# Optimization experiments

Hardware: AMD Instinct MI355X
Metric: run time of the kernel (lower is better)

## Reference

```python
import jax, jax.numpy as jnp
import numpy as np

N = 50000
E = 800000
NODE_IN = 128
HID = 256
OUT = 256
EDGE_DIM = 16
HEADS = 4
CH = HID // HEADS  # 64
NEG_SLOPE = 0.2


def _init_linear(key, fan_in, fan_out):
    k1, k2 = jax.random.split(key)
    bound = 1.0 / np.sqrt(fan_in)
    W = jax.random.uniform(k1, (fan_in, fan_out), jnp.float32, -bound, bound)
    b = jax.random.uniform(k2, (fan_out,), jnp.float32, -bound, bound)
    return W, b


def setup_inputs() -> dict:
    key = jax.random.key(0)
    ks = jax.random.split(key, 12)
    node_feats = jax.random.normal(ks[0], (N, NODE_IN), jnp.float32)
    edge_index = jax.random.randint(ks[1], (2, E), 0, N, jnp.int64)
    edge_attr = jax.random.normal(ks[2], (E, EDGE_DIM), jnp.float32)

    Wnp, bnp = _init_linear(ks[3], NODE_IN, HID)           # node_proj
    Wep, bep = _init_linear(ks[4], EDGE_DIM, HID)          # edge_proj
    # GATConv 1: in = 2*HID, out per head = CH
    Wg1, _ = _init_linear(ks[5], 2 * HID, HEADS * CH)
    as1 = jax.random.normal(ks[6], (HEADS, CH), jnp.float32) * 0.1
    ad1 = jax.random.normal(ks[7], (HEADS, CH), jnp.float32) * 0.1
    bg1 = jnp.zeros((HEADS * CH,), jnp.float32)
    # GATConv 2: in = HID, out per head = OUT//HEADS
    Wg2, _ = _init_linear(ks[8], HID, HEADS * (OUT // HEADS))
    as2 = jax.random.normal(ks[9], (HEADS, OUT // HEADS), jnp.float32) * 0.1
    ad2 = jax.random.normal(ks[10], (HEADS, OUT // HEADS), jnp.float32) * 0.1
    bg2 = jnp.zeros((OUT,), jnp.float32)
    Wo, bo = _init_linear(ks[11], OUT, OUT)                # out_proj
    return {
        "node_feats": node_feats, "edge_attr": edge_attr,
        "Wnp": Wnp, "bnp": bnp, "Wep": Wep, "bep": bep,
        "Wg1": Wg1, "as1": as1, "ad1": ad1, "bg1": bg1,
        "Wg2": Wg2, "as2": as2, "ad2": ad2, "bg2": bg2,
        "Wo": Wo, "bo": bo,
        "edge_index": edge_index,
    }


def scatter_mean(src, index, num_nodes):
    # mean of edge features grouped by target node; empty groups -> 0 (count clamped to 1)
    s = jax.ops.segment_sum(src, index, num_segments=num_nodes)
    cnt = jax.ops.segment_sum(jnp.ones((src.shape[0],), src.dtype), index, num_segments=num_nodes)
    return s / jnp.maximum(cnt, 1.0)[:, None]


def gat_conv(x, src, dst, W, att_src, att_dst, bias, num_nodes, heads, ch):
    # PyG GATConv with add_self_loops=True (loops appended by caller via src/dst),
    # concat=True, negative_slope=0.2.
    xh = (x @ W).reshape(num_nodes, heads, ch)             # [N,H,C]
    a_src = jnp.sum(xh * att_src, axis=-1)                 # [N,H]
    a_dst = jnp.sum(xh * att_dst, axis=-1)                 # [N,H]
    logits = jax.nn.leaky_relu(a_src[src] + a_dst[dst], NEG_SLOPE)  # [E,H]
    # segment softmax over incoming edges of each destination node
    m = jax.ops.segment_max(logits, dst, num_segments=num_nodes)    # [N,H]
    ex = jnp.exp(logits - m[dst])
    denom = jax.ops.segment_sum(ex, dst, num_segments=num_nodes)    # [N,H]
    alpha = ex / denom[dst]                                          # [E,H]
    msg = xh[src] * alpha[:, :, None]                                # [E,H,C]
    out = jax.ops.segment_sum(msg, dst, num_segments=num_nodes)      # [N,H,C]
    return out.reshape(num_nodes, heads * ch) + bias


def reference(node_feats, edge_attr, Wnp, bnp, Wep, bep,
              Wg1, as1, ad1, bg1, Wg2, as2, ad2, bg2, Wo, bo, edge_index):
    n = node_feats.shape[0]
    x = node_feats @ Wnp + bnp                                       # [N,HID]
    # EdgeAggregator: mean of edge_attr over target nodes, then edge_proj
    nef = scatter_mean(edge_attr, edge_index[1], n)                  # [N,EDGE_DIM]
    nef = nef @ Wep + bep                                            # [N,HID]
    x = jnp.concatenate([x, nef], axis=-1)                           # [N,2*HID]
    # add self loops once (same augmented edge set for both GAT layers)
    loops = jnp.arange(n, dtype=edge_index.dtype)
    src = jnp.concatenate([edge_index[0], loops])
    dst = jnp.concatenate([edge_index[1], loops])
    x = jax.nn.elu(gat_conv(x, src, dst, Wg1, as1, ad1, bg1, n, HEADS, CH))
    # dropout is identity in eval mode
    x = jax.nn.elu(gat_conv(x, src, dst, Wg2, as2, ad2, bg2, n, HEADS, OUT // HEADS))
    return x @ Wo + bo
```

## Files before the change

kernel.cpp:

```cpp
#include <hip/hip_runtime.h>
#include <hip/hip_bf16.h>


#define HEADS 4

typedef __attribute__((ext_vector_type(8))) _Float16 f16x8;
typedef __attribute__((ext_vector_type(4))) float f32x4;
typedef __attribute__((ext_vector_type(4))) unsigned short u16x4;
typedef __attribute__((ext_vector_type(8))) unsigned short u16x8;

__device__ __forceinline__ unsigned short f2h(float v) {
    _Float16 h = (_Float16)v;
    return __builtin_bit_cast(unsigned short, h);
}
__device__ __forceinline__ float h2f(unsigned short u) {
    return (float)__builtin_bit_cast(_Float16, u);
}
__device__ __forceinline__ void split_hilo16(float v, unsigned short& h, unsigned short& l) {
    h = f2h(v);
    l = f2h(v - h2f(h));
}
__device__ __forceinline__ void gl2lds16(const unsigned short* g, unsigned short* l) {
    __builtin_amdgcn_global_load_lds(
        (const __attribute__((address_space(1))) unsigned int*)g,
        (__attribute__((address_space(3))) unsigned int*)l,
        16, 0, 0);
}


__global__ __launch_bounds__(256) void count_kernel(
    const int* __restrict__ dst, int* __restrict__ cnt, int E)
{
    int e = blockIdx.x * 256 + threadIdx.x;
    if (e < E) atomicAdd(&cnt[dst[e]], 1);
}

__global__ __launch_bounds__(256) void scan1_kernel(
    const int* __restrict__ cnt, int* __restrict__ chunk_sum, int N)
{
    __shared__ int sd[256];
    int t = threadIdx.x;
    int n = blockIdx.x * 256 + t;
    sd[t] = (n < N) ? (cnt[n] + 1) : 0;
    __syncthreads();
    for (int o = 128; o > 0; o >>= 1) {
        if (t < o) sd[t] += sd[t + o];
        __syncthreads();
    }
    if (t == 0) chunk_sum[blockIdx.x] = sd[0];
}

__global__ __launch_bounds__(256) void scan2_kernel(
    const int* __restrict__ chunk_sum, int* __restrict__ chunk_off, int nchunk)
{
    __shared__ int sd[256];
    __shared__ int carry;
    int t = threadIdx.x;
    if (t == 0) carry = 0;
    __syncthreads();
    for (int b = 0; b < nchunk; b += 256) {
        int i = b + t;
        int v = (i < nchunk) ? chunk_sum[i] : 0;
        sd[t] = v;
        __syncthreads();
        for (int o = 1; o < 256; o <<= 1) {
            int x = (t >= o) ? sd[t - o] : 0;
            __syncthreads();
            sd[t] += x;
            __syncthreads();
        }
        if (i < nchunk) chunk_off[i] = carry + sd[t] - v;
        __syncthreads();
        if (t == 0) carry += sd[255];
        __syncthreads();
    }
}

__global__ __launch_bounds__(256) void scan3_kernel(
    const int* __restrict__ cnt, const int* __restrict__ chunk_off,
    int* __restrict__ rowptr, int* __restrict__ fillptr,
    int* __restrict__ col, int* __restrict__ eid, int N)
{
    __shared__ int sd[256];
    int t = threadIdx.x;
    int n = blockIdx.x * 256 + t;
    int v = (n < N) ? (cnt[n] + 1) : 0;
    sd[t] = v;
    __syncthreads();
    for (int o = 1; o < 256; o <<= 1) {
        int x = (t >= o) ? sd[t - o] : 0;
        __syncthreads();
        sd[t] += x;
        __syncthreads();
    }
    if (n < N) {
        int incl = sd[t];
        int r = chunk_off[blockIdx.x] + incl - v;
        rowptr[n] = r;
        col[r] = n;
        eid[r] = -1;
        fillptr[n] = r + 1;
        if (n == N - 1) rowptr[N] = chunk_off[blockIdx.x] + incl;
    }
}

__global__ __launch_bounds__(256) void fill_kernel(
    const int* __restrict__ src, const int* __restrict__ dst,
    int* __restrict__ fillptr, int* __restrict__ col, int* __restrict__ eid, int E)
{
    int e = blockIdx.x * 256 + threadIdx.x;
    if (e >= E) return;
    int d = dst[e];
    int p = atomicAdd(&fillptr[d], 1);
    col[p] = src[e];
    eid[p] = e;
}

__global__ __launch_bounds__(256) void nef_csr_kernel(
    const float* __restrict__ ea, const int* __restrict__ rowptr,
    const int* __restrict__ eid,
    unsigned short* __restrict__ AF, int N)
{
    int n = blockIdx.x * 4 + (threadIdx.x >> 6);
    if (n >= N) return;
    int t = threadIdx.x & 63;
    int f = t & 15, g = t >> 4;
    int base = rowptr[n], end = rowptr[n + 1];
    int deg = end - base - 1;
    float acc = 0.0f;
    for (int j = base + 1 + g; j < end; j += 4) {
        int e = eid[j];
        acc += ea[(size_t)e * 16 + f];
    }
    acc += __shfl_down(acc, 32, 64);
    acc += __shfl_down(acc, 16, 64);
    if (t < 16) {
        float v = acc / fmaxf((float)deg, 1.0f);
        AF[(size_t)n * 160 + 128 + t] = f2h(v);
    } else if (t < 32) {
        AF[(size_t)n * 160 + 128 + t] = 0;
    }
}

__global__ __launch_bounds__(256) void conv_f16_strided_kernel(
    const float* __restrict__ X, unsigned short* __restrict__ AF, int total)
{
    int base = (blockIdx.x * 256 + threadIdx.x) * 2;
    if (base >= total) return;
    #pragma unroll
    for (int i = 0; i < 2; i++) {
        int e = base + i;
        int row = e >> 7, c = e & 127;
        AF[(size_t)row * 160 + c] = f2h(X[e]);
    }
}

__global__ __launch_bounds__(256) void compose_w1_kernel(
    const float* __restrict__ Wnp, const float* __restrict__ Wep,
    const float* __restrict__ bnp, const float* __restrict__ bep,
    const float* __restrict__ Wg1,
    float* __restrict__ Wc, float* __restrict__ c1)
{
    int idx = blockIdx.x * 256 + threadIdx.x;
    if (idx >= 145 * 256) return;
    int i = idx >> 8, j = idx & 255;
    float s = 0.0f;
    if (i < 128) {
        for (int k = 0; k < 256; k++) s += Wnp[i * 256 + k] * Wg1[(size_t)k * 256 + j];
        Wc[i * 256 + j] = s;
    } else if (i < 144) {
        int ii = i - 128;
        for (int k = 0; k < 256; k++) s += Wep[ii * 256 + k] * Wg1[(size_t)(256 + k) * 256 + j];
        Wc[i * 256 + j] = s;
    } else {
        for (int k = 0; k < 256; k++)
            s += bnp[k] * Wg1[(size_t)k * 256 + j] + bep[k] * Wg1[(size_t)(256 + k) * 256 + j];
        c1[j] = s;
    }
}

__device__ __forceinline__ void pack_one(
    const float* __restrict__ W, int K, int KP, int idx,
    unsigned short* __restrict__ Ph, unsigned short* __restrict__ Pl)
{
    int tile = idx >> 9, w = idx & 511, lane = w >> 3, j = w & 7;
    int nk = KP >> 5;
    int ctile = tile / nk, t = tile % nk;
    int k = t * 32 + ((lane >> 4) << 3) + j;
    int n = (ctile << 4) + (lane & 15);
    float v = (k < K) ? W[(size_t)k * 256 + n] : 0.0f;
    unsigned short h, l;
    split_hilo16(v, h, l);
    Ph[idx] = h;
    Pl[idx] = l;
}

__global__ __launch_bounds__(256) void pack3_w_kernel(
    const float* __restrict__ Wc,  unsigned short* __restrict__ PcH,  unsigned short* __restrict__ PcL,
    const float* __restrict__ Wg2, unsigned short* __restrict__ Pg2H, unsigned short* __restrict__ Pg2L,
    const float* __restrict__ Wo,  unsigned short* __restrict__ PoH,  unsigned short* __restrict__ PoL)
{
    const int S0 = 160 * 256;
    const int S1 = S0 + 256 * 256;
    const int S2 = S1 + 256 * 256;
    int idx = blockIdx.x * 256 + threadIdx.x;
    if (idx < S0) {
        pack_one(Wc, 144, 160, idx, PcH, PcL);
    } else if (idx < S1) {
        pack_one(Wg2, 256, 256, idx - S0, Pg2H, Pg2L);
    } else if (idx < S2) {
        pack_one(Wo, 256, 256, idx - S1, PoH, PoL);
    }
}

template <int KSTEPS, int AMODE, int OMODE, bool FUSE_ATT>
__global__ __launch_bounds__(256, 5) void mfma_gemm_kernel(
    const unsigned short* __restrict__ Ah, const unsigned short* __restrict__ Al,
    int lda,
    const unsigned short* __restrict__ Ph, const unsigned short* __restrict__ Pl,
    const float* __restrict__ bias,
    float* __restrict__ Cf,
    unsigned short* __restrict__ Ch, unsigned short* __restrict__ Cl,
    int ldc, int col_off, int Nrows,
    const float* __restrict__ att_src, const float* __restrict__ att_dst,
    float* __restrict__ a_srcO, float* __restrict__ a_dstO)
{
    __shared__ unsigned short ldsB[2][2][8][512];
    int tid = threadIdx.x;
    int wave = tid >> 6, lane = tid & 63;
    int quad = lane >> 4, m16 = lane & 15;
    int rowblk = blockIdx.x, colhalf = blockIdx.y;
    int ctile0 = colhalf * 8;

    int row = rowblk * 64 + wave * 16 + m16;
    bool rowok = row < Nrows;
    const unsigned short* arh = Ah + (size_t)row * lda;
    const unsigned short* arl = (AMODE == 0) ? (Al + (size_t)row * lda) : nullptr;

    auto stage = [&](int t, int buf) {
        #pragma unroll
        for (int q = 0; q < 2; q++) {
            int c = wave * 2 + q;
            size_t gb = ((size_t)((ctile0 + c) * KSTEPS + t)) * 512 + lane * 8;
            gl2lds16(Ph + gb, &ldsB[buf][0][c][0]);
            gl2lds16(Pl + gb, &ldsB[buf][1][c][0]);
        }
    };
    auto loadA = [&](int t, f16x8& h, f16x8& l) {
        int k = t * 32 + quad * 8;
        h = (f16x8){};
        l = (f16x8){};
        if (rowok) {
            h = __builtin_bit_cast(f16x8, *(const u16x8*)(arh + k));
            if (AMODE == 0)
                l = __builtin_bit_cast(f16x8, *(const u16x8*)(arl + k));
        }
    };

    f32x4 acc[8] = {};
    f16x8 ah2[2], al2[2];
    loadA(0, ah2[0], al2[0]);
    stage(0, 0);
    __syncthreads();

    #pragma unroll
    for (int t = 0; t < KSTEPS; t++) {
        const int buf = t & 1;
        if (t + 1 < KSTEPS) {
            stage(t + 1, buf ^ 1);
            loadA(t + 1, ah2[(t + 1) & 1], al2[(t + 1) & 1]);
        }
        #pragma unroll
        for (int c = 0; c < 8; c++) {
            f16x8 b_h = __builtin_bit_cast(f16x8, *(const u16x8*)&ldsB[buf][0][c][lane * 8]);
            f16x8 b_l = __builtin_bit_cast(f16x8, *(const u16x8*)&ldsB[buf][1][c][lane * 8]);
            acc[c] = __builtin_amdgcn_mfma_f32_16x16x32_f16(ah2[buf], b_h, acc[c], 0, 0, 0);
            if (AMODE == 0)
                acc[c] = __builtin_amdgcn_mfma_f32_16x16x32_f16(al2[buf], b_h, acc[c], 0, 0, 0);
            acc[c] = __builtin_amdgcn_mfma_f32_16x16x32_f16(ah2[buf], b_l, acc[c], 0, 0, 0);
        }
        if (t + 1 < KSTEPS) __syncthreads();
    }

    #pragma unroll
    for (int c = 0; c < 8; c++) {
        int ocol = (ctile0 + c) * 16 + m16;
        float bv = bias ? bias[ocol] : 0.0f;
        #pragma unroll
        for (int r = 0; r < 4; r++) {
            int orow = rowblk * 64 + wave * 16 + quad * 4 + r;
            if (orow >= Nrows) continue;
            float v = acc[c][r] + bv;
            size_t oidx = (size_t)orow * ldc + col_off + ocol;
            if (OMODE == 1) {
                unsigned short h, l;
                split_hilo16(v, h, l);
                Ch[oidx] = h;
                Cl[oidx] = l;
            } else if (OMODE == 2) {
                Ch[oidx] = f2h(v);
            } else {
                Cf[oidx] = v;
            }
        }
    }

    if (FUSE_ATT) {
        float ps[4][2] = {}, pd[4][2] = {};
        #pragma unroll
        for (int c = 0; c < 8; c++) {
            int ocol = (ctile0 + c) * 16 + m16;
            float bv = bias ? bias[ocol] : 0.0f;
            float asv = att_src[ocol];
            float adv = att_dst[ocol];
            int hl = c >> 2;
            #pragma unroll
            for (int r = 0; r < 4; r++) {
                float v = acc[c][r] + bv;
                ps[r][hl] += v * asv;
                pd[r][hl] += v * adv;
            }
        }
        #pragma unroll
        for (int r = 0; r < 4; r++) {
            #pragma unroll
            for (int hl = 0; hl < 2; hl++) {
                float s = ps[r][hl], d = pd[r][hl];
                #pragma unroll
                for (int o = 8; o > 0; o >>= 1) {
                    s += __shfl_down(s, o, 64);
                    d += __shfl_down(d, o, 64);
                }
                if (m16 == 0) {
                    int orow = rowblk * 64 + wave * 16 + quad * 4 + r;
                    if (orow < Nrows) {
                        int gh = colhalf * 2 + hl;
                        a_srcO[orow * 4 + gh] = s;
                        a_dstO[orow * 4 + gh] = d;
                    }
                }
            }
        }
    }
}

template <bool OUTF16>
__global__ __launch_bounds__(256) void gat_agg_csr_kernel(
    const unsigned short* __restrict__ xh,
    const int* __restrict__ rowptr, const int* __restrict__ col,
    const float* __restrict__ a_src, const float* __restrict__ a_dst,
    const float* __restrict__ bias,
    unsigned short* __restrict__ outA, unsigned short* __restrict__ outB, int N)
{
    __shared__ float wlds[4][128][HEADS];
    int t = threadIdx.x;
    int wv = t >> 6;
    int n = blockIdx.x * 4 + wv;
    if (n >= N) return;
    int c = t & 63;
    int h = c >> 4;
    int base = rowptr[n], end = rowptr[n + 1];
    int deg = end - base;
    int e1 = end - 1;
    float4 ad = *(const float4*)&a_dst[n * 4];
    float adh = (h == 0) ? ad.x : (h == 1) ? ad.y : (h == 2) ? ad.z : ad.w;
    const unsigned short* xcol = xh + (c << 2);

    float4 acc = {0.0f, 0.0f, 0.0f, 0.0f};
    float den = 0.0f;

    if (deg <= 128) {
        float4 ds = {0.0f, 0.0f, 0.0f, 0.0f};
        for (int j = base + c; j < end; j += 64) {
            int s = col[j];
            float4 as4 = *(const float4*)&a_src[s * 4];
            float l0 = as4.x + ad.x, l1 = as4.y + ad.y;
            float l2 = as4.z + ad.z, l3 = as4.w + ad.w;
            l0 = fmaxf(l0, 0.2f * l0);
            l1 = fmaxf(l1, 0.2f * l1);
            l2 = fmaxf(l2, 0.2f * l2);
            l3 = fmaxf(l3, 0.2f * l3);
            float4 wv4 = {__expf(l0), __expf(l1), __expf(l2), __expf(l3)};
            *(float4*)&wlds[wv][j - base][0] = wv4;
            ds.x += wv4.x; ds.y += wv4.y; ds.z += wv4.z; ds.w += wv4.w;
        }
        #pragma unroll
        for (int o = 32; o > 0; o >>= 1) {
            ds.x += __shfl_down(ds.x, o, 64);
            ds.y += __shfl_down(ds.y, o, 64);
            ds.z += __shfl_down(ds.z, o, 64);
            ds.w += __shfl_down(ds.w, o, 64);
        }
        float d0 = __shfl(ds.x, 0, 64);
        float d1 = __shfl(ds.y, 0, 64);
        float d2 = __shfl(ds.z, 0, 64);
        float d3 = __shfl(ds.w, 0, 64);
        den = (h == 0) ? d0 : (h == 1) ? d1 : (h == 2) ? d2 : d3;

        for (int j = base; j < end; j += 4) {
            int j1 = j + 1 < e1 ? j + 1 : e1;
            int j2 = j + 2 < e1 ? j + 2 : e1;
            int j3 = j + 3 < e1 ? j + 3 : e1;
            int s0 = col[j], s1 = col[j1], s2 = col[j2], s3 = col[j3];
            float w0 = wlds[wv][j - base][h];
            float w1 = (j + 1 < end) ? wlds[wv][j1 - base][h] : 0.0f;
            float w2 = (j + 2 < end) ? wlds[wv][j2 - base][h] : 0.0f;
            float w3 = (j + 3 < end) ? wlds[wv][j3 - base][h] : 0.0f;
            u16x4 x0 = *(const u16x4*)(xcol + (size_t)s0 * 256);
            u16x4 x1 = *(const u16x4*)(xcol + (size_t)s1 * 256);
            u16x4 x2 = *(const u16x4*)(xcol + (size_t)s2 * 256);
            u16x4 x3 = *(const u16x4*)(xcol + (size_t)s3 * 256);
            acc.x += w0 * h2f(x0[0]) + w1 * h2f(x1[0]) + w2 * h2f(x2[0]) + w3 * h2f(x3[0]);
            acc.y += w0 * h2f(x0[1]) + w1 * h2f(x1[1]) + w2 * h2f(x2[1]) + w3 * h2f(x3[1]);
            acc.z += w0 * h2f(x0[2]) + w1 * h2f(x1[2]) + w2 * h2f(x2[2]) + w3 * h2f(x3[2]);
            acc.w += w0 * h2f(x0[3]) + w1 * h2f(x1[3]) + w2 * h2f(x2[3]) + w3 * h2f(x3[3]);
        }
    } else {
        for (int j = base; j < end; j += 4) {
            int j1 = j + 1 < e1 ? j + 1 : e1;
            int j2 = j + 2 < e1 ? j + 2 : e1;
            int j3 = j + 3 < e1 ? j + 3 : e1;
            int s0 = col[j], s1 = col[j1], s2 = col[j2], s3 = col[j3];
            float l0 = a_src[s0 * 4 + h] + adh;
            float l1 = a_src[s1 * 4 + h] + adh;
            float l2 = a_src[s2 * 4 + h] + adh;
            float l3 = a_src[s3 * 4 + h] + adh;
            l0 = fmaxf(l0, 0.2f * l0);
            l1 = fmaxf(l1, 0.2f * l1);
            l2 = fmaxf(l2, 0.2f * l2);
            l3 = fmaxf(l3, 0.2f * l3);
            float w0 = __expf(l0);
            float w1 = (j + 1 < end) ? __expf(l1) : 0.0f;
            float w2 = (j + 2 < end) ? __expf(l2) : 0.0f;
            float w3 = (j + 3 < end) ? __expf(l3) : 0.0f;
            u16x4 x0 = *(const u16x4*)(xcol + (size_t)s0 * 256);
            u16x4 x1 = *(const u16x4*)(xcol + (size_t)s1 * 256);
            u16x4 x2 = *(const u16x4*)(xcol + (size_t)s2 * 256);
            u16x4 x3 = *(const u16x4*)(xcol + (size_t)s3 * 256);
            den += (w0 + w1) + (w2 + w3);
            acc.x += w0 * h2f(x0[0]) + w1 * h2f(x1[0]) + w2 * h2f(x2[0]) + w3 * h2f(x3[0]);
            acc.y += w0 * h2f(x0[1]) + w1 * h2f(x1[1]) + w2 * h2f(x2[1]) + w3 * h2f(x3[1]);
            acc.z += w0 * h2f(x0[2]) + w1 * h2f(x1[2]) + w2 * h2f(x2[2]) + w3 * h2f(x3[2]);
            acc.w += w0 * h2f(x0[3]) + w1 * h2f(x1[3]) + w2 * h2f(x2[3]) + w3 * h2f(x3[3]);
        }
    }

    float inv = 1.0f / den;
    float4 bv = *(const float4*)(bias + (c << 2));
    float o0 = acc.x * inv + bv.x;
    float o1 = acc.y * inv + bv.y;
    float o2 = acc.z * inv + bv.z;
    float o3 = acc.w * inv + bv.w;
    o0 = (o0 > 0.0f) ? o0 : (__expf(o0) - 1.0f);
    o1 = (o1 > 0.0f) ? o1 : (__expf(o1) - 1.0f);
    o2 = (o2 > 0.0f) ? o2 : (__expf(o2) - 1.0f);
    o3 = (o3 > 0.0f) ? o3 : (__expf(o3) - 1.0f);
    if (OUTF16) {
        u16x4 H;
        H[0] = f2h(o0); H[1] = f2h(o1); H[2] = f2h(o2); H[3] = f2h(o3);
        *(u16x4*)(&outA[(size_t)n * 256 + (c << 2)]) = H;
    } else {
        u16x4 H, L;
        split_hilo16(o0, ((unsigned short*)&H)[0], ((unsigned short*)&L)[0]);
        split_hilo16(o1, ((unsigned short*)&H)[1], ((unsigned short*)&L)[1]);
        split_hilo16(o2, ((unsigned short*)&H)[2], ((unsigned short*)&L)[2]);
        split_hilo16(o3, ((unsigned short*)&H)[3], ((unsigned short*)&L)[3]);
        *(u16x4*)(&outA[(size_t)n * 256 + (c << 2)]) = H;
        *(u16x4*)(&outB[(size_t)n * 256 + (c << 2)]) = L;
    }
}


extern "C" void kernel_launch(void* const* d_in, const int* in_sizes, int n_in,
                              void* d_out, int out_size, void* d_ws, size_t ws_size,
                              hipStream_t stream)
{
    const float* node_feats = (const float*)d_in[0];
    const float* edge_attr  = (const float*)d_in[1];
    const float* Wnp = (const float*)d_in[2];
    const float* bnp = (const float*)d_in[3];
    const float* Wep = (const float*)d_in[4];
    const float* bep = (const float*)d_in[5];
    const float* Wg1 = (const float*)d_in[6];
    const float* as1 = (const float*)d_in[7];
    const float* ad1 = (const float*)d_in[8];
    const float* bg1 = (const float*)d_in[9];
    const float* Wg2 = (const float*)d_in[10];
    const float* as2 = (const float*)d_in[11];
    const float* ad2 = (const float*)d_in[12];
    const float* bg2 = (const float*)d_in[13];
    const float* Wo  = (const float*)d_in[14];
    const float* bo  = (const float*)d_in[15];
    const int*   ei  = (const int*)d_in[16];

    const int N = in_sizes[0] / 128;
    const int E = in_sizes[16] / 2;
    const int* src = ei;
    const int* dst = ei + E;
    const int nchunk = (N + 255) / 256;
    const int EN = E + N;

    typedef unsigned short u16;

    char* base = (char*)d_ws;
    size_t off = 0;
    auto alloc = [&](size_t bytes) -> char* {
        char* p = base + off;
        off += (bytes + 255) & ~(size_t)255;
        return p;
    };
    u16* xhh = (u16*)alloc((size_t)N * 256 * 2);
    u16* R2  = (u16*)alloc((size_t)N * 512 * 2);
    u16* R3  = (u16*)alloc((size_t)N * 512 * 2);
    float* a_src = (float*)alloc((size_t)N * 4 * 4);
    float* a_dst = (float*)alloc((size_t)N * 4 * 4);
    float* Wc    = (float*)alloc(144 * 256 * 4);
    float* c1    = (float*)alloc(256 * 4);
    u16* PcH  = (u16*)alloc(160 * 256 * 2);
    u16* PcL  = (u16*)alloc(160 * 256 * 2);
    u16* Pg2H = (u16*)alloc(256 * 256 * 2);
    u16* Pg2L = (u16*)alloc(256 * 256 * 2);
    u16* PoH  = (u16*)alloc(256 * 256 * 2);
    u16* PoL  = (u16*)alloc(256 * 256 * 2);
    int* cnt       = (int*)alloc((size_t)N * 4);
    int* rowptr    = (int*)alloc((size_t)(N + 1) * 4);
    int* fillptr   = (int*)alloc((size_t)N * 4);
    int* chunk_sum = (int*)alloc((size_t)nchunk * 4);
    int* chunk_off = (int*)alloc((size_t)nchunk * 4);
    int* colv      = (int*)alloc((size_t)EN * 4);
    int* eid       = (int*)alloc((size_t)EN * 4);

    u16* AcatF = R2;
    u16* x3F   = R2;
    u16* x4H = R3;
    u16* x4L = R3 + (size_t)N * 256;

    float* out = (float*)d_out;
    dim3 ggrid((N + 63) / 64, 2);

    hipMemsetAsync(cnt, 0, (size_t)N * sizeof(int), stream);
    count_kernel<<<(E + 255) / 256, 256, 0, stream>>>(dst, cnt, E);
    scan1_kernel<<<nchunk, 256, 0, stream>>>(cnt, chunk_sum, N);
    scan2_kernel<<<1, 256, 0, stream>>>(chunk_sum, chunk_off, nchunk);
    scan3_kernel<<<nchunk, 256, 0, stream>>>(cnt, chunk_off, rowptr, fillptr, colv, eid, N);
    fill_kernel<<<(E + 255) / 256, 256, 0, stream>>>(src, dst, fillptr, colv, eid, E);

    nef_csr_kernel<<<(N + 3) / 4, 256, 0, stream>>>(edge_attr, rowptr, eid, AcatF, N);
    conv_f16_strided_kernel<<<((N * 128) / 2 + 255) / 256, 256, 0, stream>>>(
        node_feats, AcatF, N * 128);
    compose_w1_kernel<<<145, 256, 0, stream>>>(Wnp, Wep, bnp, bep, Wg1, Wc, c1);
    {
        const int total = 160 * 256 + 256 * 256 + 256 * 256;
        pack3_w_kernel<<<(total + 255) / 256, 256, 0, stream>>>(
            Wc, PcH, PcL, Wg2, Pg2H, Pg2L, Wo, PoH, PoL);
    }

    mfma_gemm_kernel<5, 1, 2, true><<<ggrid, 256, 0, stream>>>(
        AcatF, nullptr, 160, PcH, PcL, c1, nullptr, xhh, nullptr, 256, 0, N,
        as1, ad1, a_src, a_dst);
    gat_agg_csr_kernel<true><<<(N + 3) / 4, 256, 0, stream>>>(
        xhh, rowptr, colv, a_src, a_dst, bg1, x3F, nullptr, N);

    mfma_gemm_kernel<8, 1, 2, true><<<ggrid, 256, 0, stream>>>(
        x3F, nullptr, 256, Pg2H, Pg2L, nullptr, nullptr, xhh, nullptr, 256, 0, N,
        as2, ad2, a_src, a_dst);
    gat_agg_csr_kernel<false><<<(N + 3) / 4, 256, 0, stream>>>(
        xhh, rowptr, colv, a_src, a_dst, bg2, x4H, x4L, N);

    mfma_gemm_kernel<8, 0, 0, false><<<ggrid, 256, 0, stream>>>(
        x4H, x4L, 256, PoH, PoL, bo, out, nullptr, nullptr, 256, 0, N,
        nullptr, nullptr, nullptr, nullptr);
}
```

Before: 539.0 us.

## Fuse fp32-to-fp16 input conversion into first GEMM and preload A fragments

Removes the separate conversion kernel that wrote node features as fp16 into a strided concat buffer. The first GEMM now reads fp32 node features directly and converts them in registers, and reads edge-mean features from a small separate buffer. All GEMMs now preload every A fragment for the whole K range into registers up front, and launch bounds drop to 4 blocks per SM to make room. This saves a full write-and-read pass over the feature matrix, at the cost of more registers and lower occupancy in all GEMMs.

New measurement: 533.1 us (median of 2 runs). About the same (-1.1%).

```diff
diff --git a/kernel.cpp b/kernel.cpp
--- a/kernel.cpp
+++ b/kernel.cpp
@@ -119,7 +119,7 @@
 __global__ __launch_bounds__(256) void nef_csr_kernel(
     const float* __restrict__ ea, const int* __restrict__ rowptr,
     const int* __restrict__ eid,
-    unsigned short* __restrict__ AF, int N)
+    unsigned short* __restrict__ nefF, int N)
 {
     int n = blockIdx.x * 4 + (threadIdx.x >> 6);
     if (n >= N) return;
@@ -136,22 +136,9 @@
     acc += __shfl_down(acc, 16, 64);
     if (t < 16) {
         float v = acc / fmaxf((float)deg, 1.0f);
-        AF[(size_t)n * 160 + 128 + t] = f2h(v);
+        nefF[(size_t)n * 32 + t] = f2h(v);
     } else if (t < 32) {
-        AF[(size_t)n * 160 + 128 + t] = 0;
-    }
-}
-
-__global__ __launch_bounds__(256) void conv_f16_strided_kernel(
-    const float* __restrict__ X, unsigned short* __restrict__ AF, int total)
-{
-    int base = (blockIdx.x * 256 + threadIdx.x) * 2;
-    if (base >= total) return;
-    #pragma unroll
-    for (int i = 0; i < 2; i++) {
-        int e = base + i;
-        int row = e >> 7, c = e & 127;
-        AF[(size_t)row * 160 + c] = f2h(X[e]);
+        nefF[(size_t)n * 32 + t] = 0;
     }
 }
 
@@ -214,8 +201,9 @@
 }
 
 template <int KSTEPS, int AMODE, int OMODE, bool FUSE_ATT>
-__global__ __launch_bounds__(256, 5) void mfma_gemm_kernel(
+__global__ __launch_bounds__(256, 4) void mfma_gemm_kernel(
     const unsigned short* __restrict__ Ah, const unsigned short* __restrict__ Al,
+    const float* __restrict__ Af32,
     int lda,
     const unsigned short* __restrict__ Ph, const unsigned short* __restrict__ Pl,
     const float* __restrict__ bias,
@@ -234,8 +222,6 @@
 
     int row = rowblk * 64 + wave * 16 + m16;
     bool rowok = row < Nrows;
-    const unsigned short* arh = Ah + (size_t)row * lda;
-    const unsigned short* arl = (AMODE == 0) ? (Al + (size_t)row * lda) : nullptr;
 
     auto stage = [&](int t, int buf) {
         #pragma unroll
@@ -246,38 +232,65 @@
             gl2lds16(Pl + gb, &ldsB[buf][1][c][0]);
         }
     };
-    auto loadA = [&](int t, f16x8& h, f16x8& l) {
-        int k = t * 32 + quad * 8;
-        h = (f16x8){};
-        l = (f16x8){};
-        if (rowok) {
-            h = __builtin_bit_cast(f16x8, *(const u16x8*)(arh + k));
-            if (AMODE == 0)
-                l = __builtin_bit_cast(f16x8, *(const u16x8*)(arl + k));
-        }
-    };
+
+    u16x8 aH[KSTEPS];
+    u16x8 aL[AMODE == 0 ? KSTEPS : 1];
+    f32x4 aF[AMODE == 3 ? 2 * KSTEPS : 1];
+    #pragma unroll
+    for (int t = 0; t < KSTEPS; t++) {
+        if (AMODE == 3) {
+            if (t < KSTEPS - 1) {
+                aF[2 * t] = (f32x4){};
+                aF[2 * t + 1] = (f32x4){};
+                if (rowok) {
+                    const float* p = Af32 + (size_t)row * 128 + t * 32 + quad * 8;
+                    aF[2 * t]     = *(const f32x4*)p;
+                    aF[2 * t + 1] = *(const f32x4*)(p + 4);
+                }
+            } else {
+                aH[t] = (u16x8){};
+                if (rowok) aH[t] = *(const u16x8*)(Ah + (size_t)row * 32 + quad * 8);
+            }
+        } else {
+            int k = t * 32 + quad * 8;
+            aH[t] = (u16x8){};
+            if (rowok) aH[t] = *(const u16x8*)(Ah + (size_t)row * lda + k);
+            if (AMODE == 0) {
+                aL[t] = (u16x8){};
+                if (rowok) aL[t] = *(const u16x8*)(Al + (size_t)row * lda + k);
+            }
+        }
+    }
 
     f32x4 acc[8] = {};
-    f16x8 ah2[2], al2[2];
-    loadA(0, ah2[0], al2[0]);
     stage(0, 0);
     __syncthreads();
 
     #pragma unroll
     for (int t = 0; t < KSTEPS; t++) {
         const int buf = t & 1;
-        if (t + 1 < KSTEPS) {
-            stage(t + 1, buf ^ 1);
-            loadA(t + 1, ah2[(t + 1) & 1], al2[(t + 1) & 1]);
-        }
+        if (t + 1 < KSTEPS) stage(t + 1, buf ^ 1);
+
+        f16x8 a_h, a_l;
+        if (AMODE == 3 && t < KSTEPS - 1) {
+            #pragma unroll
+            for (int i = 0; i < 4; i++) {
+                ((_Float16*)&a_h)[i]     = (_Float16)aF[2 * t][i];
+                ((_Float16*)&a_h)[4 + i] = (_Float16)aF[2 * t + 1][i];
+            }
+        } else {
+            a_h = __builtin_bit_cast(f16x8, aH[t]);
+        }
+        if (AMODE == 0) a_l = __builtin_bit_cast(f16x8, aL[t]);
+
         #pragma unroll
         for (int c = 0; c < 8; c++) {
             f16x8 b_h = __builtin_bit_cast(f16x8, *(const u16x8*)&ldsB[buf][0][c][lane * 8]);
             f16x8 b_l = __builtin_bit_cast(f16x8, *(const u16x8*)&ldsB[buf][1][c][lane * 8]);
-            acc[c] = __builtin_amdgcn_mfma_f32_16x16x32_f16(ah2[buf], b_h, acc[c], 0, 0, 0);
+            acc[c] = __builtin_amdgcn_mfma_f32_16x16x32_f16(a_h, b_h, acc[c], 0, 0, 0);
             if (AMODE == 0)
-                acc[c] = __builtin_amdgcn_mfma_f32_16x16x32_f16(al2[buf], b_h, acc[c], 0, 0, 0);
-            acc[c] = __builtin_amdgcn_mfma_f32_16x16x32_f16(ah2[buf], b_l, acc[c], 0, 0, 0);
+                acc[c] = __builtin_amdgcn_mfma_f32_16x16x32_f16(a_l, b_h, acc[c], 0, 0, 0);
+            acc[c] = __builtin_amdgcn_mfma_f32_16x16x32_f16(a_h, b_l, acc[c], 0, 0, 0);
         }
         if (t + 1 < KSTEPS) __syncthreads();
     }
@@ -509,9 +522,10 @@
         off += (bytes + 255) & ~(size_t)255;
         return p;
     };
-    u16* xhh = (u16*)alloc((size_t)N * 256 * 2);
-    u16* R2  = (u16*)alloc((size_t)N * 512 * 2);
-    u16* R3  = (u16*)alloc((size_t)N * 512 * 2);
+    u16* xhh  = (u16*)alloc((size_t)N * 256 * 2);
+    u16* x3F  = (u16*)alloc((size_t)N * 256 * 2);
+    u16* R3   = (u16*)alloc((size_t)N * 512 * 2);
+    u16* nefF = (u16*)alloc((size_t)N * 32 * 2);
     float* a_src = (float*)alloc((size_t)N * 4 * 4);
     float* a_dst = (float*)alloc((size_t)N * 4 * 4);
     float* Wc    = (float*)alloc(144 * 256 * 4);
@@ -530,8 +544,6 @@
     int* colv      = (int*)alloc((size_t)EN * 4);
     int* eid       = (int*)alloc((size_t)EN * 4);
 
-    u16* AcatF = R2;
-    u16* x3F   = R2;
     u16* x4H = R3;
     u16* x4L = R3 + (size_t)N * 256;
 
@@ -545,9 +557,7 @@
     scan3_kernel<<<nchunk, 256, 0, stream>>>(cnt, chunk_off, rowptr, fillptr, colv, eid, N);
     fill_kernel<<<(E + 255) / 256, 256, 0, stream>>>(src, dst, fillptr, colv, eid, E);
 
-    nef_csr_kernel<<<(N + 3) / 4, 256, 0, stream>>>(edge_attr, rowptr, eid, AcatF, N);
-    conv_f16_strided_kernel<<<((N * 128) / 2 + 255) / 256, 256, 0, stream>>>(
-        node_feats, AcatF, N * 128);
+    nef_csr_kernel<<<(N + 3) / 4, 256, 0, stream>>>(edge_attr, rowptr, eid, nefF, N);
     compose_w1_kernel<<<145, 256, 0, stream>>>(Wnp, Wep, bnp, bep, Wg1, Wc, c1);
     {
         const int total = 160 * 256 + 256 * 256 + 256 * 256;
@@ -555,19 +565,19 @@
             Wc, PcH, PcL, Wg2, Pg2H, Pg2L, Wo, PoH, PoL);
     }
 
-    mfma_gemm_kernel<5, 1, 2, true><<<ggrid, 256, 0, stream>>>(
-        AcatF, nullptr, 160, PcH, PcL, c1, nullptr, xhh, nullptr, 256, 0, N,
-        as1, ad1, a_src, a_dst);
+    mfma_gemm_kernel<5, 3, 2, true><<<ggrid, 256, 0, stream>>>(
+        nefF, nullptr, node_feats, 160, PcH, PcL, c1, nullptr, xhh, nullptr,
+        256, 0, N, as1, ad1, a_src, a_dst);
     gat_agg_csr_kernel<true><<<(N + 3) / 4, 256, 0, stream>>>(
         xhh, rowptr, colv, a_src, a_dst, bg1, x3F, nullptr, N);
 
     mfma_gemm_kernel<8, 1, 2, true><<<ggrid, 256, 0, stream>>>(
-        x3F, nullptr, 256, Pg2H, Pg2L, nullptr, nullptr, xhh, nullptr, 256, 0, N,
-        as2, ad2, a_src, a_dst);
+        x3F, nullptr, nullptr, 256, Pg2H, Pg2L, nullptr, nullptr, xhh, nullptr,
+        256, 0, N, as2, ad2, a_src, a_dst);
     gat_agg_csr_kernel<false><<<(N + 3) / 4, 256, 0, stream>>>(
         xhh, rowptr, colv, a_src, a_dst, bg2, x4H, x4L, N);
 
     mfma_gemm_kernel<8, 0, 0, false><<<ggrid, 256, 0, stream>>>(
-        x4H, x4L, 256, PoH, PoL, bo, out, nullptr, nullptr, 256, 0, N,
-        nullptr, nullptr, nullptr, nullptr);
-}
+        x4H, x4L, nullptr, 256, PoH, PoL, bo, out, nullptr, nullptr,
+        256, 0, N, nullptr, nullptr, nullptr, nullptr);
+}
```
